# Kernel tuning notes

Hardware: AMD Instinct MI355X
Metric: run time of the kernel (lower is better)

The kernel has to match this reference:

```python
import jax, jax.numpy as jnp
import numpy as np

SIGMA = 25.0
EPS = 1e-5
TWO_PI = 2.0 * np.pi


def _gn(x, gamma, beta, groups):
    # GroupNorm over (C//G, H, W) per group, per-channel affine.
    B, C, H, W = x.shape
    xg = x.reshape(B, groups, -1)
    m = xg.mean(-1, keepdims=True)
    v = xg.var(-1, keepdims=True)
    xn = ((xg - m) * jax.lax.rsqrt(v + EPS)).reshape(B, C, H, W)
    return xn * gamma[None, :, None, None] + beta[None, :, None, None]


def _conv3(x, k, b):
    y = jax.lax.conv_general_dilated(x, k, (1, 1), 'SAME',
                                     dimension_numbers=('NCHW', 'OIHW', 'NCHW'))
    return y + b[None, :, None, None]


def _tconv2(x, k, b):
    # ConvTranspose2d kernel=2 stride=2 (no overlap) == einsum + reshape.
    # k: [C_in, C_out, 2, 2]
    B, C, H, W = x.shape
    O = k.shape[1]
    y = jnp.einsum('bchw,codq->bohdwq', x, k).reshape(B, O, 2 * H, 2 * W)
    return y + b[None, :, None, None]


def _conv1(x, k, b):
    # 1x1 conv; k: [C_out, C_in]
    return jnp.einsum('bchw,oc->bohw', x, k) + b[None, :, None, None]


def _pool(x):
    B, C, H, W = x.shape
    return x.reshape(B, C, H // 2, 2, W // 2, 2).max(axis=(3, 5))


def _std(t):
    return jnp.sqrt((SIGMA ** (2.0 * t) - 1.0) / (2.0 * jnp.log(SIGMA)))


def setup_inputs() -> dict:
    key = jax.random.key(0)
    ks = jax.random.split(key, 16)
    B, H, W = 64, 128, 128
    E = 2 * W  # 256 = embed_dim

    def w(k, shape, fan_in):
        return jax.random.normal(k, shape, jnp.float32) / np.sqrt(fan_in)

    inp = {
        'x': jax.random.normal(ks[0], (B, 1, H, W), jnp.float32),
        't': jax.random.uniform(ks[1], (B,), jnp.float32, 1e-3, 1.0),
        'Wf': jax.random.normal(ks[2], (H, W), jnp.float32) * 30.0,  # fixed Fourier features
        'fc1_w': w(ks[3], (E, E), E),
        'fc1_b': jnp.zeros((E,), jnp.float32),
        'conv1_k': w(ks[4], (6, 1, 3, 3), 9),
        'conv1_b': jnp.zeros((6,), jnp.float32),
        'gn1_g': jnp.ones((6,), jnp.float32), 'gn1_b': jnp.zeros((6,), jnp.float32),
        'conv2_k': w(ks[5], (24, 6, 3, 3), 6 * 9),
        'conv2_b': jnp.zeros((24,), jnp.float32),
        'gn2_g': jnp.ones((24,), jnp.float32), 'gn2_b': jnp.zeros((24,), jnp.float32),
        't3_k': w(ks[6], (24, 24, 2, 2), 24 * 4),
        't3_b': jnp.zeros((24,), jnp.float32),
        'gn3_g': jnp.ones((48,), jnp.float32), 'gn3_b': jnp.zeros((48,), jnp.float32),
        't4_k': w(ks[7], (48, 12, 2, 2), 48 * 4),
        't4_b': jnp.zeros((12,), jnp.float32),
        'gn4_g': jnp.ones((18,), jnp.float32), 'gn4_b': jnp.zeros((18,), jnp.float32),
        't5_k': w(ks[8], (6, 18), 18),
        't5_b': jnp.zeros((6,), jnp.float32),
        'gn5_g': jnp.ones((6,), jnp.float32), 'gn5_b': jnp.zeros((6,), jnp.float32),
        'fin_k': w(ks[9], (1, 6), 6),
        'fin_b': jnp.zeros((1,), jnp.float32),
    }
    return inp


def reference(x, t, Wf, fc1_w, fc1_b, conv1_k, conv1_b, gn1_g, gn1_b,
              conv2_k, conv2_b, gn2_g, gn2_b, t3_k, t3_b, gn3_g, gn3_b,
              t4_k, t4_b, gn4_g, gn4_b, t5_k, t5_b, gn5_g, gn5_b,
              fin_k, fin_b):
    # Vectorized Gaussian Fourier projection: [B,1,H,W] -> [B,1,H,2W]
    p = x * Wf[None, None] * TWO_PI
    xe = jnp.concatenate([jnp.sin(p), jnp.cos(p)], axis=-1)
    # fc1 on last dim (embed_dim = 2W)
    xf = jnp.einsum('bchw,ow->bcho', xe, fc1_w) + fc1_b
    c1 = _conv3(xf, conv1_k, conv1_b)                              # [B,6,H,2W]
    p1 = _pool(jax.nn.relu(_gn(c1, gn1_g, gn1_b, 6)))              # [B,6,H/2,W]
    c2 = _conv3(p1, conv2_k, conv2_b)                              # [B,24,H/2,W]
    p2 = _pool(jax.nn.relu(_gn(c2, gn2_g, gn2_b, 24)))             # [B,24,H/4,W/2]
    a = p2 * jax.nn.sigmoid(p2)                                    # SiLU bottleneck
    u3 = _tconv2(a, t3_k, t3_b)                                    # [B,24,H/2,W]
    g3 = _gn(jnp.concatenate([c2, u3], axis=1), gn3_g, gn3_b, 6)   # 48 ch
    u4 = _tconv2(g3, t4_k, t4_b)                                   # [B,12,H,2W]
    g4 = _gn(jnp.concatenate([c1, u4], axis=1), gn4_g, gn4_b, 6)   # 18 ch
    u5 = _conv1(g4, t5_k, t5_b)                                    # [B,6,H,2W]
    g5 = _gn(u5, gn5_g, gn5_b, 6)
    return _conv1(g5, fin_k, fin_b) / _std(t)[:, None, None, None]
```

## Files before the change

kernel.cpp:

```cpp
#include <hip/hip_runtime.h>
#include <hip/hip_bf16.h>
#include <math.h>

#define BB 64
#define HH 128
#define WW 128
#define EE 256
#define HP (HH*EE)
#define H2 64
#define W2 128
#define PL2 (H2*W2)
#define H4 32
#define W4 64
#define PL4 (H4*W4)

typedef __hip_bfloat16 bf;
typedef unsigned short ushortt;
typedef __attribute__((ext_vector_type(8))) __bf16 b8v;
typedef __attribute__((ext_vector_type(4))) float f4v;

__device__ __forceinline__ float tof(bf v)    { return __bfloat162float(v); }
__device__ __forceinline__ bf    tob(float v) { return __float2bfloat16(v); }
__device__ __forceinline__ unsigned int bfbits(float v) {
    return (unsigned int)__builtin_bit_cast(ushortt, __float2bfloat16(v));
}
__device__ __forceinline__ float b2f(unsigned int u16) {
    unsigned int x = u16 << 16;
    return __builtin_bit_cast(float, x);
}
__device__ __forceinline__ void wred2(float& s, float& q) {
    #pragma unroll
    for (int m = 32; m; m >>= 1) {
        s += __shfl_xor(s, m);
        q += __shfl_xor(q, m);
    }
}
__device__ __forceinline__ void wred2_32(float& s, float& q) {
    #pragma unroll
    for (int m = 16; m; m >>= 1) {
        s += __shfl_xor(s, m);
        q += __shfl_xor(q, m);
    }
}

__global__ __launch_bounds__(256) void k_fourier_fc1(
    const float* __restrict__ x, const float* __restrict__ Wf,
    const float* __restrict__ fc1_w, const float* __restrict__ fc1_b,
    bf* __restrict__ xf, float* __restrict__ mb)
{
    __shared__ ushortt sA[64*264];
    __shared__ ushortt sB[64*264];
    int t = threadIdx.x;
    for (int i = blockIdx.x*256 + t; i < 9216; i += 512*256) mb[i] = 0.f;
    int rb = blockIdx.x >> 2, cb = blockIdx.x & 3;
    int row0 = rb*64, col0 = cb*64;
    const float TP = 6.2831853071795864769f;
    for (int it = 0; it < 32; ++it) {
        int i = it*256 + t;
        int r = i >> 7, w = i & 127;
        int rg = row0 + r;
        float p = x[(size_t)rg*WW + w] * Wf[(size_t)(rg & (HH-1))*WW + w] * TP;
        sA[r*264 + w]       = (ushortt)bfbits(__sinf(p));
        sA[r*264 + 128 + w] = (ushortt)bfbits(__cosf(p));
    }
    #pragma unroll
    for (int it = 0; it < 16; ++it) {
        int i = it*256 + t;
        int o = i >> 6, c4 = i & 63;
        float4 w4 = *(const float4*)(fc1_w + (size_t)(col0 + o)*EE + c4*4);
        uint2 pk;
        pk.x = bfbits(w4.x) | (bfbits(w4.y) << 16);
        pk.y = bfbits(w4.z) | (bfbits(w4.w) << 16);
        *(uint2*)&sB[o*264 + c4*4] = pk;
    }
    __syncthreads();
    int lane = t & 63, wid = t >> 6;
    int m = lane & 15, kq = (lane >> 4) * 8;
    f4v acc[4] = {};
    const ushortt* aBase = &sA[(wid*16 + m)*264 + kq];
    #pragma unroll
    for (int k0 = 0; k0 < 8; ++k0) {
        b8v av = *(const b8v*)(aBase + k0*32);
        #pragma unroll
        for (int t4 = 0; t4 < 4; ++t4) {
            b8v bv = *(const b8v*)&sB[(t4*16 + m)*264 + k0*32 + kq];
            acc[t4] = __builtin_amdgcn_mfma_f32_16x16x32_bf16(av, bv, acc[t4], 0, 0, 0);
        }
    }
    int rbase = row0 + wid*16 + (lane >> 4)*4;
    #pragma unroll
    for (int t4 = 0; t4 < 4; ++t4) {
        int col = col0 + t4*16 + m;
        float bias = fc1_b[col];
        #pragma unroll
        for (int r = 0; r < 4; ++r)
            xf[(size_t)(rbase + r)*EE + col] = tob(acc[t4][r] + bias);
    }
}

__global__ __launch_bounds__(256) void k_conv1(
    const bf* __restrict__ xf, const float* __restrict__ k,
    const float* __restrict__ bias, bf* __restrict__ c1, float* __restrict__ mc1)
{
    __shared__ ushortt sT[6*272];
    __shared__ float red[4][6][2];
    int t = threadIdx.x;
    int ht = blockIdx.x & 31, b = blockIdx.x >> 5;
    int h0 = ht*4;
    const bf* src = xf + (size_t)b*HP;
    if (t < 192) {
        int r = t >> 5, i = t & 31;
        int gy = h0 - 1 + r;
        uint4 v = {0,0,0,0};
        if (gy >= 0 && gy < HH) v = *(const uint4*)(src + (size_t)gy*EE + i*8);
        *(uint4*)&sT[r*272 + 8 + i*8] = v;
    } else if (t < 204) {
        int e = t - 192;
        int r = e >> 1, s = e & 1;
        uint4 z = {0,0,0,0};
        *(uint4*)&sT[r*272 + s*264] = z;
    }
    __syncthreads();
    int wq = (t & 63)*4, hl = t >> 6;
    int lane = t & 63, wid = t >> 6;
    float v[3][6];
    #pragma unroll
    for (int ky = 0; ky < 3; ++ky)
      #pragma unroll
      for (int j = 0; j < 6; ++j)
        v[ky][j] = b2f((unsigned)sT[(hl+ky)*272 + 7 + wq + j]);
    int h = h0 + hl;
    #pragma unroll
    for (int o = 0; o < 6; ++o) {
        float bv = bias[o];
        float a0=bv, a1=bv, a2=bv, a3=bv;
        #pragma unroll
        for (int ky = 0; ky < 3; ++ky)
          #pragma unroll
          for (int kx = 0; kx < 3; ++kx) {
            float wv = k[o*9 + ky*3 + kx];
            a0 += v[ky][kx+0]*wv;
            a1 += v[ky][kx+1]*wv;
            a2 += v[ky][kx+2]*wv;
            a3 += v[ky][kx+3]*wv;
          }
        uint2 pk;
        pk.x = bfbits(a0) | (bfbits(a1) << 16);
        pk.y = bfbits(a2) | (bfbits(a3) << 16);
        *(uint2*)(c1 + ((size_t)(b*6+o)*HH + h)*EE + wq) = pk;
        float s = a0+a1+a2+a3, q = a0*a0+a1*a1+a2*a2+a3*a3;
        wred2(s, q);
        if (lane == 0) { red[wid][o][0] = s; red[wid][o][1] = q; }
    }
    __syncthreads();
    if (t < 6) {
        float S = 0.f, Q = 0.f;
        #pragma unroll
        for (int wv = 0; wv < 4; ++wv) { S += red[wv][t][0]; Q += red[wv][t][1]; }
        atomicAdd(&mc1[((size_t)b*6 + t)*2],     S);
        atomicAdd(&mc1[((size_t)b*6 + t)*2 + 1], Q);
    }
}

__global__ __launch_bounds__(256) void k_conv2(
    const bf* __restrict__ c1, const float* __restrict__ mc1,
    const float* __restrict__ g1, const float* __restrict__ be1,
    const float* __restrict__ kw, const float* __restrict__ bias,
    bf* __restrict__ c2, float* __restrict__ mc2)
{
    __shared__ ushortt sA[256*72];
    __shared__ ushortt sW[32*72];
    __shared__ ushortt sP[6*4*136];
    __shared__ float ssl[12];
    __shared__ float redS[24], redQ[24];
    int t = threadIdx.x;
    int ht = blockIdx.x & 31, b = blockIdx.x >> 5;
    int h0 = ht*2;
    int lane = t & 63, wid = t >> 6;
    if (t < 24) { redS[t] = 0.f; redQ[t] = 0.f; }
    if (t < 6) {
        float s = mc1[((size_t)b*6 + t)*2], q = mc1[((size_t)b*6 + t)*2 + 1];
        float mean = s * (1.f/HP);
        float var  = q * (1.f/HP) - mean*mean;
        float rstd = rsqrtf(var + 1e-5f);
        float sc = g1[t]*rstd;
        ssl[t*2] = sc; ssl[t*2+1] = be1[t] - mean*sc;
    }
    for (int i = t; i < 1152; i += 256) ((unsigned*)sW)[i] = 0;
    __syncthreads();
    for (int i = t; i < 3120; i += 256) {
        int c = i / 520, rem = i % 520;
        int ry = rem / 130, rx = rem % 130;
        int gy = h0 - 1 + ry, gx = rx - 1;
        float v = 0.f;
        if (gy >= 0 && gy < H2 && gx >= 0 && gx < W2) {
            const bf* pp = c1 + ((size_t)(b*6+c)*HH + 2*gy)*EE + 2*gx;
            unsigned r0 = *(const unsigned*)pp;
            unsigned r1 = *(const unsigned*)(pp + EE);
            float sc = ssl[c*2], sh = ssl[c*2+1];
            float e0 = fmaxf(b2f(r0 & 0xffff)*sc+sh, 0.f);
            float e1 = fmaxf(b2f(r0 >> 16)   *sc+sh, 0.f);
            float e2 = fmaxf(b2f(r1 & 0xffff)*sc+sh, 0.f);
            float e3 = fmaxf(b2f(r1 >> 16)   *sc+sh, 0.f);
            v = fmaxf(fmaxf(e0,e1), fmaxf(e2,e3));
        }
        sP[c*544 + ry*136 + rx] = (ushortt)bfbits(v);
    }
    for (int e = t; e < 1296; e += 256) {
        int o = e / 54, kk = e % 54;
        sW[o*72 + kk] = (ushortt)bfbits(kw[e]);
    }
    __syncthreads();
    {
        int r = t >> 7, xx = t & 127;
        unsigned u[32];
        #pragma unroll
        for (int p = 0; p < 27; ++p) {
            int k0 = 2*p, k1 = 2*p + 1;
            int c0 = k0/9, y0 = (k0%9)/3, x0 = k0%3;
            int c1i = k1/9, y1 = (k1%9)/3, x1 = k1%3;
            unsigned lo = sP[c0*544 + (r+y0)*136 + xx + x0];
            unsigned hi = sP[c1i*544 + (r+y1)*136 + xx + x1];
            u[p] = lo | (hi << 16);
        }
        #pragma unroll
        for (int p = 27; p < 32; ++p) u[p] = 0;
        #pragma unroll
        for (int e = 0; e < 8; ++e) {
            uint4 pk; pk.x = u[4*e]; pk.y = u[4*e+1]; pk.z = u[4*e+2]; pk.w = u[4*e+3];
            *(uint4*)&sA[t*72 + e*8] = pk;
        }
    }
    __syncthreads();
    int m = lane & 15, kq = (lane >> 4)*8;
    b8v wv[2][2];
    #pragma unroll
    for (int nt = 0; nt < 2; ++nt)
      #pragma unroll
      for (int ks = 0; ks < 2; ++ks)
        wv[nt][ks] = *(const b8v*)&sW[(nt*16 + m)*72 + ks*32 + kq];
    f4v acc[4][2] = {};
    #pragma unroll
    for (int mt = 0; mt < 4; ++mt) {
        const ushortt* ab = &sA[(wid*64 + mt*16 + m)*72 + kq];
        b8v a0 = *(const b8v*)(ab);
        b8v a1 = *(const b8v*)(ab + 32);
        #pragma unroll
        for (int nt = 0; nt < 2; ++nt) {
            acc[mt][nt] = __builtin_amdgcn_mfma_f32_16x16x32_bf16(a0, wv[nt][0], acc[mt][nt], 0, 0, 0);
            acc[mt][nt] = __builtin_amdgcn_mfma_f32_16x16x32_bf16(a1, wv[nt][1], acc[mt][nt], 0, 0, 0);
        }
    }
    __syncthreads();
    ushortt* sC = sA;
    int q4 = lane >> 4;
    #pragma unroll
    for (int mt = 0; mt < 4; ++mt) {
        int pxb = wid*64 + mt*16 + q4*4;
        #pragma unroll
        for (int nt = 0; nt < 2; ++nt) {
            int o = nt*16 + m;
            if (o < 24) {
                float bo = bias[o];
                #pragma unroll
                for (int r = 0; r < 4; ++r) {
                    int px = pxb + r;
                    sC[o*272 + (px >> 7)*136 + (px & 127)] =
                        (ushortt)bfbits(acc[mt][nt][r] + bo);
                }
            }
        }
    }
    __syncthreads();
    #pragma unroll
    for (int j = 0; j < 3; ++j) {
        int idx = j*256 + t;
        int o = idx >> 5;
        int rem = idx & 31;
        int r = rem >> 4, x8 = (rem & 15)*8;
        uint4 v = *(const uint4*)&sC[o*272 + r*136 + x8];
        *(uint4*)(c2 + ((size_t)(b*24+o)*H2 + h0 + r)*W2 + x8) = v;
        float v0 = b2f(v.x & 0xffff), v1 = b2f(v.x >> 16);
        float v2 = b2f(v.y & 0xffff), v3 = b2f(v.y >> 16);
        float v4 = b2f(v.z & 0xffff), v5 = b2f(v.z >> 16);
        float v6 = b2f(v.w & 0xffff), v7 = b2f(v.w >> 16);
        float s = v0+v1+v2+v3+v4+v5+v6+v7;
        float qv = v0*v0+v1*v1+v2*v2+v3*v3+v4*v4+v5*v5+v6*v6+v7*v7;
        wred2_32(s, qv);
        if ((lane & 31) == 0) { atomicAdd(&redS[o], s); atomicAdd(&redQ[o], qv); }
    }
    __syncthreads();
    if (t < 24) {
        atomicAdd(&mc2[((size_t)b*24 + t)*2],     redS[t]);
        atomicAdd(&mc2[((size_t)b*24 + t)*2 + 1], redQ[t]);
    }
}

__global__ __launch_bounds__(256) void k_tconv3(
    const bf* __restrict__ c2, const float* __restrict__ mc2,
    const float* __restrict__ g2, const float* __restrict__ be2,
    const float* __restrict__ k3, const float* __restrict__ b3,
    bf* __restrict__ u3, float* __restrict__ mu3)
{
    __shared__ ushortt sBuf[27648];
    __shared__ float redS[24], redQ[24];
    __shared__ float ssl[48];
    ushortt* sA = sBuf;
    ushortt* sW = sBuf + 10240;
    int t = threadIdx.x;
    int b = blockIdx.x >> 3, pg = blockIdx.x & 7;
    int lane = t & 63, wid = t >> 6;
    if (t < 24) {
        redS[t] = 0.f; redQ[t] = 0.f;
        float s = mc2[((size_t)b*24 + t)*2], q = mc2[((size_t)b*24 + t)*2 + 1];
        float mean = s * (1.f/PL2);
        float var  = q * (1.f/PL2) - mean*mean;
        float rstd = rsqrtf(var + 1e-5f);
        float sc = g2[t]*rstd;
        ssl[t*2] = sc; ssl[t*2+1] = be2[t] - mean*sc;
    }
    #pragma unroll
    for (int j = 0; j < 9; ++j) {
        int e = j*256 + t;
        int c = e / 96, n = e % 96;
        sW[n*40 + c] = (ushortt)bfbits(k3[e]);
    }
    if (t < 96) { uint4 z = {0,0,0,0}; *(uint4*)&sW[t*40 + 24] = z; }
    { uint4 z = {0,0,0,0}; *(uint4*)&sA[t*40 + 24] = z; }
    __syncthreads();
    #pragma unroll
    for (int j = 0; j < 12; ++j) {
        int i = j*256 + t;
        int c = i >> 7, pr = i & 127;
        int px0 = pr*2;
        int h4 = (pg*256 + px0) >> 6, w4 = px0 & 63;
        const bf* pp = c2 + ((size_t)b*24 + c)*PL2 + (size_t)(2*h4)*W2 + 2*w4;
        uint2 r0 = *(const uint2*)pp;
        uint2 r1 = *(const uint2*)(pp + W2);
        float sc = ssl[c*2], sh = ssl[c*2+1];
        float e0 = fmaxf(b2f(r0.x & 0xffff)*sc+sh, 0.f);
        float e1 = fmaxf(b2f(r0.x >> 16)   *sc+sh, 0.f);
        float f0 = fmaxf(b2f(r1.x & 0xffff)*sc+sh, 0.f);
        float f1 = fmaxf(b2f(r1.x >> 16)   *sc+sh, 0.f);
        float m0 = fmaxf(fmaxf(e0,e1), fmaxf(f0,f1));
        m0 = m0 / (1.f + expf(-m0));
        float e2 = fmaxf(b2f(r0.y & 0xffff)*sc+sh, 0.f);
        float e3 = fmaxf(b2f(r0.y >> 16)   *sc+sh, 0.f);
        float f2 = fmaxf(b2f(r1.y & 0xffff)*sc+sh, 0.f);
        float f3 = fmaxf(b2f(r1.y >> 16)   *sc+sh, 0.f);
        float m1 = fmaxf(fmaxf(e2,e3), fmaxf(f2,f3));
        m1 = m1 / (1.f + expf(-m1));
        sA[px0*40 + c]     = (ushortt)bfbits(m0);
        sA[(px0+1)*40 + c] = (ushortt)bfbits(m1);
    }
    __syncthreads();
    int m = lane & 15, kq = (lane >> 4)*8;
    b8v wv[6];
    #pragma unroll
    for (int nt = 0; nt < 6; ++nt)
        wv[nt] = *(const b8v*)&sW[(nt*16 + m)*40 + kq];
    f4v acc[4][6] = {};
    #pragma unroll
    for (int mt = 0; mt < 4; ++mt) {
        b8v av = *(const b8v*)&sA[(wid*64 + mt*16 + m)*40 + kq];
        #pragma unroll
        for (int nt = 0; nt < 6; ++nt)
            acc[mt][nt] = __builtin_amdgcn_mfma_f32_16x16x32_bf16(av, wv[nt], acc[mt][nt], 0, 0, 0);
    }
    __syncthreads();
    ushortt* sC = sBuf;
    int q4 = lane >> 4;
    #pragma unroll
    for (int mt = 0; mt < 4; ++mt) {
        int pxb = wid*64 + mt*16 + q4*4;
        #pragma unroll
        for (int nt = 0; nt < 6; ++nt) {
            int n = nt*16 + m;
            int o = n >> 2, d = (n >> 1) & 1, qq = n & 1;
            float bo = b3[o];
            #pragma unroll
            for (int r = 0; r < 4; ++r) {
                int px = pxb + r;
                int yl = ((px >> 6) << 1) + d;
                int xx = ((px & 63) << 1) + qq;
                sC[o*1152 + yl*144 + xx] = (ushortt)bfbits(acc[mt][nt][r] + bo);
            }
        }
    }
    __syncthreads();
    bf* outb = u3 + (size_t)b*24*PL2;
    #pragma unroll
    for (int j = 0; j < 12; ++j) {
        int idx = j*256 + t;
        int o = idx >> 7;
        int rem = idx & 127;
        int yl = rem >> 4, xc = (rem & 15)*8;
        uint4 v = *(const uint4*)&sC[o*1152 + yl*144 + xc];
        *(uint4*)(outb + ((size_t)o*H2 + pg*8 + yl)*W2 + xc) = v;
        float v0 = b2f(v.x & 0xffff), v1 = b2f(v.x >> 16);
        float v2 = b2f(v.y & 0xffff), v3 = b2f(v.y >> 16);
        float v4 = b2f(v.z & 0xffff), v5 = b2f(v.z >> 16);
        float v6 = b2f(v.w & 0xffff), v7 = b2f(v.w >> 16);
        float s = v0+v1+v2+v3+v4+v5+v6+v7;
        float qv = v0*v0+v1*v1+v2*v2+v3*v3+v4*v4+v5*v5+v6*v6+v7*v7;
        wred2(s, qv);
        if (lane == 0) { atomicAdd(&redS[o], s); atomicAdd(&redQ[o], qv); }
    }
    __syncthreads();
    if (t < 24) {
        atomicAdd(&mu3[((size_t)b*24 + t)*2],     redS[t]);
        atomicAdd(&mu3[((size_t)b*24 + t)*2 + 1], redQ[t]);
    }
}

__global__ __launch_bounds__(256) void k_tconv4(
    const bf* __restrict__ c2, const bf* __restrict__ u3,
    const float* __restrict__ mc2, const float* __restrict__ mu3,
    const float* __restrict__ g3, const float* __restrict__ be3,
    const float* __restrict__ k4, const float* __restrict__ bias4,
    bf* __restrict__ u4, float* __restrict__ mu4)
{
    __shared__ ushortt sA[256*72];
    __shared__ ushortt sW[48*72];
    __shared__ float redS[12], redQ[12];
    __shared__ float ssl[96];
    int t = threadIdx.x;
    int b = blockIdx.x >> 5, pg = blockIdx.x & 31;
    int lane = t & 63, wid = t >> 6;
    if (t < 12) { redS[t] = 0.f; redQ[t] = 0.f; }
    if (t < 6) {
        float s = 0.f, q = 0.f;
        #pragma unroll
        for (int cl = 0; cl < 8; ++cl) {
            int gc = t*8 + cl;
            const float* p = (gc < 24) ? mc2 + ((size_t)b*24 + gc)*2
                                       : mu3 + ((size_t)b*24 + gc - 24)*2;
            s += p[0]; q += p[1];
        }
        float inv_n = 1.f/((float)PL2*8.f);
        float mean = s*inv_n;
        float var  = q*inv_n - mean*mean;
        float rstd = rsqrtf(var + 1e-5f);
        #pragma unroll
        for (int cl = 0; cl < 8; ++cl) {
            int gc = t*8 + cl;
            float sc = g3[gc]*rstd;
            ssl[gc*2] = sc; ssl[gc*2+1] = be3[gc] - mean*sc;
        }
    }
    #pragma unroll
    for (int j = 0; j < 9; ++j) {
        int e = j*256 + t;
        if (e < 2304) {
            int c = e / 48, n = e % 48;
            sW[n*72 + c] = (ushortt)bfbits(k4[e]);
        }
    }
    if (t < 96) {
        uint4 z = {0,0,0,0};
        int n = t >> 1, c0 = 48 + (t & 1)*8;
        *(uint4*)&sW[n*72 + c0] = z;
    }
    __syncthreads();
    {
        int pix = pg*256 + t;
        const bf* c2p = c2 + (size_t)b*24*PL2 + pix;
        const bf* u3p = u3 + (size_t)b*24*PL2 + pix;
        ushortt* row = &sA[t*72];
        #pragma unroll
        for (int g = 0; g < 6; ++g) {
            unsigned pr[4];
            #pragma unroll
            for (int hc = 0; hc < 4; ++hc) {
                int c0 = g*8 + hc*2;
                float r0 = (c0 < 24) ? tof(c2p[(size_t)c0*PL2]) : tof(u3p[(size_t)(c0-24)*PL2]);
                float r1 = (c0+1 < 24) ? tof(c2p[(size_t)(c0+1)*PL2]) : tof(u3p[(size_t)(c0+1-24)*PL2]);
                float v0 = r0 * ssl[2*c0]   + ssl[2*c0+1];
                float v1 = r1 * ssl[2*c0+2] + ssl[2*c0+3];
                pr[hc] = bfbits(v0) | (bfbits(v1) << 16);
            }
            uint4 pk; pk.x = pr[0]; pk.y = pr[1]; pk.z = pr[2]; pk.w = pr[3];
            *(uint4*)&row[g*8] = pk;
        }
        uint4 z = {0,0,0,0};
        *(uint4*)&row[48] = z;
        *(uint4*)&row[56] = z;
    }
    __syncthreads();
    int m = lane & 15, kq = (lane >> 4)*8;
    b8v bfr[3][2];
    #pragma unroll
    for (int nt = 0; nt < 3; ++nt)
      #pragma unroll
      for (int ks = 0; ks < 2; ++ks)
        bfr[nt][ks] = *(const b8v*)&sW[(nt*16 + m)*72 + ks*32 + kq];
    f4v acc[4][3] = {};
    #pragma unroll
    for (int mt = 0; mt < 4; ++mt) {
        const ushortt* ab = &sA[(wid*64 + mt*16 + m)*72 + kq];
        b8v a0 = *(const b8v*)(ab);
        b8v a1 = *(const b8v*)(ab + 32);
        #pragma unroll
        for (int nt = 0; nt < 3; ++nt) {
            acc[mt][nt] = __builtin_amdgcn_mfma_f32_16x16x32_bf16(a0, bfr[nt][0], acc[mt][nt], 0, 0, 0);
            acc[mt][nt] = __builtin_amdgcn_mfma_f32_16x16x32_bf16(a1, bfr[nt][1], acc[mt][nt], 0, 0, 0);
        }
    }
    __syncthreads();
    ushortt* sC = sA;
    int q4 = lane >> 4;
    #pragma unroll
    for (int mt = 0; mt < 4; ++mt) {
        int pxb = wid*64 + mt*16 + q4*4;
        #pragma unroll
        for (int nt = 0; nt < 3; ++nt) {
            int n = nt*16 + m;
            int o = n >> 2, d = (n >> 1) & 1, qq = n & 1;
            float bo = bias4[o];
            #pragma unroll
            for (int r = 0; r < 4; ++r) {
                int px = pxb + r;
                int yl = ((px >> 7) << 1) + d;
                int xx = ((px & 127) << 1) + qq;
                sC[o*1024 + yl*256 + xx] = (ushortt)bfbits(acc[mt][nt][r] + bo);
            }
        }
    }
    __syncthreads();
    {
        bf* outb = u4 + (size_t)b*12*HP;
        #pragma unroll
        for (int j = 0; j < 6; ++j) {
            int idx16 = j*256 + t;
            int el = idx16*8;
            int o = el >> 10, rem = el & 1023, yl = rem >> 8, x0 = rem & 255;
            uint4 v = *(const uint4*)&sC[el];
            *(uint4*)(outb + ((size_t)o*HH + pg*4 + yl)*EE + x0) = v;
            float v0 = b2f(v.x & 0xffff), v1 = b2f(v.x >> 16);
            float v2 = b2f(v.y & 0xffff), v3 = b2f(v.y >> 16);
            float v4 = b2f(v.z & 0xffff), v5 = b2f(v.z >> 16);
            float v6 = b2f(v.w & 0xffff), v7 = b2f(v.w >> 16);
            float s = v0+v1+v2+v3+v4+v5+v6+v7;
            float qv = v0*v0+v1*v1+v2*v2+v3*v3+v4*v4+v5*v5+v6*v6+v7*v7;
            wred2(s, qv);
            if (lane == 0) { atomicAdd(&redS[o], s); atomicAdd(&redQ[o], qv); }
        }
    }
    __syncthreads();
    if (t < 12) {
        atomicAdd(&mu4[((size_t)b*12 + t)*2],     redS[t]);
        atomicAdd(&mu4[((size_t)b*12 + t)*2 + 1], redQ[t]);
    }
}

__global__ __launch_bounds__(256) void k_conv1x1_u5(
    const bf* __restrict__ c1, const bf* __restrict__ u4,
    const float* __restrict__ mc1, const float* __restrict__ mu4,
    const float* __restrict__ g4, const float* __restrict__ be4,
    const float* __restrict__ k, const float* __restrict__ bias,
    bf* __restrict__ u5, float* __restrict__ mu5)
{
    __shared__ float red[4][6][2];
    __shared__ float ssl[36];
    int t = threadIdx.x;
    int b  = blockIdx.x >> 4;
    int pg = blockIdx.x & 15;
    int pix = pg*2048 + t*8;
    int lane = t & 63, wid = t >> 6;
    if (t < 6) {
        float s = 0.f, q = 0.f;
        #pragma unroll
        for (int cl = 0; cl < 3; ++cl) {
            int gc = t*3 + cl;
            const float* p = (gc < 6) ? mc1 + ((size_t)b*6 + gc)*2
                                      : mu4 + ((size_t)b*12 + gc - 6)*2;
            s += p[0]; q += p[1];
        }
        float inv_n = 1.f/((float)HP*3.f);
        float mean = s*inv_n;
        float var  = q*inv_n - mean*mean;
        float rstd = rsqrtf(var + 1e-5f);
        #pragma unroll
        for (int cl = 0; cl < 3; ++cl) {
            int gc = t*3 + cl;
            float sc = g4[gc]*rstd;
            ssl[gc*2] = sc; ssl[gc*2+1] = be4[gc] - mean*sc;
        }
    }
    __syncthreads();
    const bf* c1p = c1 + ((size_t)b*6)*HP + pix;
    const bf* u4p = u4 + ((size_t)b*12)*HP + pix;
    float acc[6][8];
    #pragma unroll
    for (int o = 0; o < 6; ++o) {
        float bv = bias[o];
        #pragma unroll
        for (int j = 0; j < 8; ++j) acc[o][j] = bv;
    }
    #pragma unroll
    for (int c = 0; c < 18; ++c) {
        uint4 r = (c < 6) ? *(const uint4*)(c1p + (size_t)c*HP)
                          : *(const uint4*)(u4p + (size_t)(c-6)*HP);
        float sc = ssl[2*c], sh = ssl[2*c+1];
        float v[8];
        v[0] = b2f(r.x & 0xffff)*sc + sh;  v[1] = b2f(r.x >> 16)*sc + sh;
        v[2] = b2f(r.y & 0xffff)*sc + sh;  v[3] = b2f(r.y >> 16)*sc + sh;
        v[4] = b2f(r.z & 0xffff)*sc + sh;  v[5] = b2f(r.z >> 16)*sc + sh;
        v[6] = b2f(r.w & 0xffff)*sc + sh;  v[7] = b2f(r.w >> 16)*sc + sh;
        #pragma unroll
        for (int o = 0; o < 6; ++o) {
            float wv = k[o*18 + c];
            #pragma unroll
            for (int j = 0; j < 8; ++j) acc[o][j] += v[j]*wv;
        }
    }
    #pragma unroll
    for (int o = 0; o < 6; ++o) {
        uint4 pk;
        pk.x = bfbits(acc[o][0]) | (bfbits(acc[o][1]) << 16);
        pk.y = bfbits(acc[o][2]) | (bfbits(acc[o][3]) << 16);
        pk.z = bfbits(acc[o][4]) | (bfbits(acc[o][5]) << 16);
        pk.w = bfbits(acc[o][6]) | (bfbits(acc[o][7]) << 16);
        *(uint4*)(u5 + ((size_t)(b*6+o))*HP + pix) = pk;
        float s = 0.f, q = 0.f;
        #pragma unroll
        for (int j = 0; j < 8; ++j) { s += acc[o][j]; q += acc[o][j]*acc[o][j]; }
        wred2(s, q);
        if (lane == 0) { red[wid][o][0] = s; red[wid][o][1] = q; }
    }
    __syncthreads();
    if (t < 6) {
        float S = 0.f, Q = 0.f;
        #pragma unroll
        for (int wv = 0; wv < 4; ++wv) { S += red[wv][t][0]; Q += red[wv][t][1]; }
        atomicAdd(&mu5[((size_t)b*6 + t)*2],     S);
        atomicAdd(&mu5[((size_t)b*6 + t)*2 + 1], Q);
    }
}

__global__ __launch_bounds__(256) void k_final(
    const bf* __restrict__ u5, const float* __restrict__ mu5,
    const float* __restrict__ g5, const float* __restrict__ be5,
    const float* __restrict__ k, const float* __restrict__ bias,
    const float* __restrict__ t, float* __restrict__ out)
{
    __shared__ float ssl[12];
    int tt = threadIdx.x;
    int b = blockIdx.x >> 4;
    int pix = ((blockIdx.x & 15)*256 + tt)*8;
    if (tt < 6) {
        float s = mu5[((size_t)b*6 + tt)*2], q = mu5[((size_t)b*6 + tt)*2 + 1];
        float mean = s * (1.f/HP);
        float var  = q * (1.f/HP) - mean*mean;
        float rstd = rsqrtf(var + 1e-5f);
        float sc = g5[tt]*rstd;
        ssl[tt*2] = sc; ssl[tt*2+1] = be5[tt] - mean*sc;
    }
    __syncthreads();
    const bf* up = u5 + (size_t)b*6*HP + pix;
    float bv = bias[0];
    float a[8];
    #pragma unroll
    for (int j = 0; j < 8; ++j) a[j] = bv;
    #pragma unroll
    for (int c = 0; c < 6; ++c) {
        uint4 r = *(const uint4*)(up + (size_t)c*HP);
        float sc = ssl[2*c], sh = ssl[2*c+1];
        float wv = k[c];
        a[0] += (b2f(r.x & 0xffff)*sc + sh) * wv;
        a[1] += (b2f(r.x >> 16)   *sc + sh) * wv;
        a[2] += (b2f(r.y & 0xffff)*sc + sh) * wv;
        a[3] += (b2f(r.y >> 16)   *sc + sh) * wv;
        a[4] += (b2f(r.z & 0xffff)*sc + sh) * wv;
        a[5] += (b2f(r.z >> 16)   *sc + sh) * wv;
        a[6] += (b2f(r.w & 0xffff)*sc + sh) * wv;
        a[7] += (b2f(r.w >> 16)   *sc + sh) * wv;
    }
    float tb = t[b];
    const float lns = 3.2188758248682007492f;
    float var = (expf(2.f*tb*lns) - 1.f) / (2.f*lns);
    float rs = rsqrtf(var);
    float4 o0; o0.x = a[0]*rs; o0.y = a[1]*rs; o0.z = a[2]*rs; o0.w = a[3]*rs;
    float4 o1; o1.x = a[4]*rs; o1.y = a[5]*rs; o1.z = a[6]*rs; o1.w = a[7]*rs;
    float* op = out + (size_t)b*HP + pix;
    *(float4*)op       = o0;
    *(float4*)(op + 4) = o1;
}

extern "C" void kernel_launch(void* const* d_in, const int* in_sizes, int n_in,
                              void* d_out, int out_size, void* d_ws, size_t ws_size,
                              hipStream_t stream)
{
    const float* x       = (const float*)d_in[0];
    const float* t       = (const float*)d_in[1];
    const float* Wf      = (const float*)d_in[2];
    const float* fc1_w   = (const float*)d_in[3];
    const float* fc1_b   = (const float*)d_in[4];
    const float* conv1_k = (const float*)d_in[5];
    const float* conv1_b = (const float*)d_in[6];
    const float* gn1_g   = (const float*)d_in[7];
    const float* gn1_b   = (const float*)d_in[8];
    const float* conv2_k = (const float*)d_in[9];
    const float* conv2_b = (const float*)d_in[10];
    const float* gn2_g   = (const float*)d_in[11];
    const float* gn2_b   = (const float*)d_in[12];
    const float* t3_k    = (const float*)d_in[13];
    const float* t3_b    = (const float*)d_in[14];
    const float* gn3_g   = (const float*)d_in[15];
    const float* gn3_b   = (const float*)d_in[16];
    const float* t4_k    = (const float*)d_in[17];
    const float* t4_b    = (const float*)d_in[18];
    const float* gn4_g   = (const float*)d_in[19];
    const float* gn4_b   = (const float*)d_in[20];
    const float* t5_k    = (const float*)d_in[21];
    const float* t5_b    = (const float*)d_in[22];
    const float* gn5_g   = (const float*)d_in[23];
    const float* gn5_b   = (const float*)d_in[24];
    const float* fin_k   = (const float*)d_in[25];
    const float* fin_b   = (const float*)d_in[26];

    bf* wsb = (bf*)d_ws;
    bf* c1 = wsb;
    bf* c2 = wsb + 12582912;
    bf* u3 = wsb + 25165824;
    bf* u4 = wsb + 37748736;
    bf* xf = wsb + 39845888;
    bf* u5 = wsb + 12582912;
    float* mb = (float*)(wsb + 62914560);
    float* mc1 = mb;
    float* mc2 = mb + 768;
    float* mu3 = mb + 3840;
    float* mu4 = mb + 6912;
    float* mu5 = mb + 8448;

    k_fourier_fc1<<<512, 256, 0, stream>>>(x, Wf, fc1_w, fc1_b, xf, mb);
    k_conv1<<<2048, 256, 0, stream>>>(xf, conv1_k, conv1_b, c1, mc1);
    k_conv2<<<2048, 256, 0, stream>>>(c1, mc1, gn1_g, gn1_b,
                                      conv2_k, conv2_b, c2, mc2);
    k_tconv3<<<512, 256, 0, stream>>>(c2, mc2, gn2_g, gn2_b,
                                      t3_k, t3_b, u3, mu3);
    k_tconv4<<<2048, 256, 0, stream>>>(c2, u3, mc2, mu3, gn3_g, gn3_b,
                                       t4_k, t4_b, u4, mu4);
    k_conv1x1_u5<<<1024, 256, 0, stream>>>(c1, u4, mc1, mu4, gn4_g, gn4_b,
                                           t5_k, t5_b, u5, mu5);
    k_final<<<1024, 256, 0, stream>>>(u5, mu5, gn5_g, gn5_b,
                                      fin_k, fin_b, t, (float*)d_out);
}
```

Baseline: 248.7 us.

## Swizzle tconv4 LDS tiles and store MFMA results directly to global

```diff
diff --git a/kernel.cpp b/kernel.cpp
--- a/kernel.cpp
+++ b/kernel.cpp
@@ -420,13 +420,14 @@
     const float* __restrict__ k4, const float* __restrict__ bias4,
     bf* __restrict__ u4, float* __restrict__ mu4)
 {
-    __shared__ ushortt sA[256*72];
-    __shared__ ushortt sW[48*72];
+    __shared__ ushortt sA[256*64];
+    __shared__ ushortt sW[48*64];
     __shared__ float redS[12], redQ[12];
     __shared__ float ssl[96];
     int t = threadIdx.x;
     int b = blockIdx.x >> 5, pg = blockIdx.x & 31;
     int lane = t & 63, wid = t >> 6;
+    int m = lane & 15, q4 = lane >> 4;
     if (t < 12) { redS[t] = 0.f; redQ[t] = 0.f; }
     if (t < 6) {
         float s = 0.f, q = 0.f;
@@ -451,22 +452,19 @@
     #pragma unroll
     for (int j = 0; j < 9; ++j) {
         int e = j*256 + t;
-        if (e < 2304) {
-            int c = e / 48, n = e % 48;
-            sW[n*72 + c] = (ushortt)bfbits(k4[e]);
-        }
+        int c = e / 48, n = e % 48;
+        sW[n*64 + ((((c >> 3) ^ (n & 7)) << 3) | (c & 7))] = (ushortt)bfbits(k4[e]);
     }
     if (t < 96) {
         uint4 z = {0,0,0,0};
-        int n = t >> 1, c0 = 48 + (t & 1)*8;
-        *(uint4*)&sW[n*72 + c0] = z;
-    }
-    __syncthreads();
+        int n = t >> 1, kb = 6 + (t & 1);
+        *(uint4*)&sW[n*64 + ((kb ^ (n & 7)) << 3)] = z;
+    }
     {
-        int pix = pg*256 + t;
+        int px = t;
+        int pix = pg*256 + px;
         const bf* c2p = c2 + (size_t)b*24*PL2 + pix;
         const bf* u3p = u3 + (size_t)b*24*PL2 + pix;
-        ushortt* row = &sA[t*72];
         #pragma unroll
         for (int g = 0; g < 6; ++g) {
             unsigned pr[4];
@@ -480,70 +478,74 @@
                 pr[hc] = bfbits(v0) | (bfbits(v1) << 16);
             }
             uint4 pk; pk.x = pr[0]; pk.y = pr[1]; pk.z = pr[2]; pk.w = pr[3];
-            *(uint4*)&row[g*8] = pk;
+            *(uint4*)&sA[px*64 + ((g ^ (px & 7)) << 3)] = pk;
         }
         uint4 z = {0,0,0,0};
-        *(uint4*)&row[48] = z;
-        *(uint4*)&row[56] = z;
-    }
-    __syncthreads();
-    int m = lane & 15, kq = (lane >> 4)*8;
+        *(uint4*)&sA[px*64 + ((6 ^ (px & 7)) << 3)] = z;
+        *(uint4*)&sA[px*64 + ((7 ^ (px & 7)) << 3)] = z;
+    }
+    __syncthreads();
     b8v bfr[3][2];
     #pragma unroll
-    for (int nt = 0; nt < 3; ++nt)
-      #pragma unroll
-      for (int ks = 0; ks < 2; ++ks)
-        bfr[nt][ks] = *(const b8v*)&sW[(nt*16 + m)*72 + ks*32 + kq];
+    for (int nt = 0; nt < 3; ++nt) {
+        int n = nt*16 + m;
+        #pragma unroll
+        for (int ks = 0; ks < 2; ++ks)
+            bfr[nt][ks] = *(const b8v*)&sW[n*64 + (((ks*4 + q4) ^ (n & 7)) << 3)];
+    }
     f4v acc[4][3] = {};
     #pragma unroll
     for (int mt = 0; mt < 4; ++mt) {
-        const ushortt* ab = &sA[(wid*64 + mt*16 + m)*72 + kq];
-        b8v a0 = *(const b8v*)(ab);
-        b8v a1 = *(const b8v*)(ab + 32);
+        int px = wid*64 + mt*16 + m;
+        b8v a0 = *(const b8v*)&sA[px*64 + (((q4)     ^ (px & 7)) << 3)];
+        b8v a1 = *(const b8v*)&sA[px*64 + (((4 + q4) ^ (px & 7)) << 3)];
         #pragma unroll
         for (int nt = 0; nt < 3; ++nt) {
             acc[mt][nt] = __builtin_amdgcn_mfma_f32_16x16x32_bf16(a0, bfr[nt][0], acc[mt][nt], 0, 0, 0);
             acc[mt][nt] = __builtin_amdgcn_mfma_f32_16x16x32_bf16(a1, bfr[nt][1], acc[mt][nt], 0, 0, 0);
         }
     }
-    __syncthreads();
-    ushortt* sC = sA;
-    int q4 = lane >> 4;
-    #pragma unroll
-    for (int mt = 0; mt < 4; ++mt) {
-        int pxb = wid*64 + mt*16 + q4*4;
-        #pragma unroll
-        for (int nt = 0; nt < 3; ++nt) {
-            int n = nt*16 + m;
-            int o = n >> 2, d = (n >> 1) & 1, qq = n & 1;
-            float bo = bias4[o];
+    float sAcc[3] = {0.f, 0.f, 0.f}, qAcc[3] = {0.f, 0.f, 0.f};
+    int qq = m & 1;
+    #pragma unroll
+    for (int nt = 0; nt < 3; ++nt) {
+        int n = nt*16 + m;
+        int o = n >> 2, d = (n >> 1) & 1;
+        float bo = bias4[o];
+        #pragma unroll
+        for (int mt = 0; mt < 4; ++mt) {
+            int pxb = wid*64 + mt*16 + q4*4;
+            unsigned wds[4];
+            float s = 0.f, q = 0.f;
             #pragma unroll
             for (int r = 0; r < 4; ++r) {
-                int px = pxb + r;
-                int yl = ((px >> 7) << 1) + d;
-                int xx = ((px & 127) << 1) + qq;
-                sC[o*1024 + yl*256 + xx] = (ushortt)bfbits(acc[mt][nt][r] + bo);
+                float v = acc[mt][nt][r] + bo;
+                float vp = __shfl_xor(v, 1);
+                unsigned lo = bfbits(v), hi = bfbits(vp);
+                wds[r] = lo | (hi << 16);
+                float f0 = b2f(lo), f1 = b2f(hi);
+                s += f0 + f1;
+                q += f0*f0 + f1*f1;
             }
-        }
-    }
-    __syncthreads();
-    {
-        bf* outb = u4 + (size_t)b*12*HP;
-        #pragma unroll
-        for (int j = 0; j < 6; ++j) {
-            int idx16 = j*256 + t;
-            int el = idx16*8;
-            int o = el >> 10, rem = el & 1023, yl = rem >> 8, x0 = rem & 255;
-            uint4 v = *(const uint4*)&sC[el];
-            *(uint4*)(outb + ((size_t)o*HH + pg*4 + yl)*EE + x0) = v;
-            float v0 = b2f(v.x & 0xffff), v1 = b2f(v.x >> 16);
-            float v2 = b2f(v.y & 0xffff), v3 = b2f(v.y >> 16);
-            float v4 = b2f(v.z & 0xffff), v5 = b2f(v.z >> 16);
-            float v6 = b2f(v.w & 0xffff), v7 = b2f(v.w >> 16);
-            float s = v0+v1+v2+v3+v4+v5+v6+v7;
-            float qv = v0*v0+v1*v1+v2*v2+v3*v3+v4*v4+v5*v5+v6*v6+v7*v7;
-            wred2(s, qv);
-            if (lane == 0) { atomicAdd(&redS[o], s); atomicAdd(&redQ[o], qv); }
+            if (qq == 0) {
+                int h2 = (pg*256 + pxb) >> 7;
+                int w0 = pxb & 127;
+                uint4 pk; pk.x = wds[0]; pk.y = wds[1]; pk.z = wds[2]; pk.w = wds[3];
+                *(uint4*)(u4 + (((size_t)(b*12 + o))*HH + 2*h2 + d)*EE + 2*w0) = pk;
+                sAcc[nt] += s; qAcc[nt] += q;
+            }
+        }
+    }
+    #pragma unroll
+    for (int nt = 0; nt < 3; ++nt) {
+        float s = sAcc[nt], q = qAcc[nt];
+        s += __shfl_xor(s, 2);  q += __shfl_xor(q, 2);
+        s += __shfl_xor(s, 16); q += __shfl_xor(q, 16);
+        s += __shfl_xor(s, 32); q += __shfl_xor(q, 32);
+        if ((lane & 51) == 0) {
+            int o = nt*4 + (m >> 2);
+            atomicAdd(&redS[o], s);
+            atomicAdd(&redQ[o], q);
         }
     }
     __syncthreads();
```

Result: faster. 236.6 us (-4.9%).
